# Kernel tuning notes

Measured on AMD Instinct MI355X. Metric: run time of the kernel, lower is better.

Reference implementation:

```python
import jax, jax.numpy as jnp
import numpy as np

G, A = 512, 24            # graphs, atoms per graph (constant -> static edge count)
N, E = G * A, G * A * A   # nodes, fully-connected edges per graph (incl. self loops)
HID, TDIM, BB, NFREQ, NLAYER = 128, 256, 64, 10, 4
DIS = NFREQ * 2 * 3                     # SinusoidsEmbedding dim = 60
EDGE_IN = 2 * HID + 6 + DIS             # 322
LAT_IN = HID + 16 + TDIM                # 400


def setup_inputs() -> dict:
    key = jax.random.key(0)
    ks = jax.random.split(key, 32)
    s = 0.02

    # block-diagonal fully-connected edge list (dense_to_sparse of ones(A,A) per graph)
    local = np.arange(A)
    off = np.repeat(np.arange(G) * A, A * A)
    e0 = np.tile(np.repeat(local, A), G) + off   # row index
    e1 = np.tile(np.tile(local, A), G) + off     # col index
    edge_index = jnp.asarray(np.stack([e0, e1]), dtype=jnp.int32)

    inp = {
        "t": jax.random.normal(ks[0], (G, TDIM), jnp.float32),
        "bb_embs": jax.random.normal(ks[1], (N, BB), jnp.float32),
        "frac_coords": jax.random.uniform(ks[2], (N, 3), jnp.float32),
        "so3_vecs": jax.random.normal(ks[3], (N, 16), jnp.float32),
        "lattices": jax.random.normal(ks[4], (G, 6), jnp.float32),
        "num_atoms": jnp.full((G,), A, dtype=jnp.int32),
        "node2graph": jnp.repeat(jnp.arange(G, dtype=jnp.int32), A),
        "edge_index": edge_index,
        # parameters
        "W_emb": jax.random.normal(ks[5], (BB, HID)) * s,
        "b_emb": jnp.zeros((HID,), jnp.float32),
        "W_lat": jax.random.normal(ks[6], (LAT_IN, HID)) * s,
        "b_lat": jnp.zeros((HID,), jnp.float32),
        "We1": jax.random.normal(ks[7], (NLAYER, EDGE_IN, HID)) * s,
        "be1": jnp.zeros((NLAYER, HID), jnp.float32),
        "We2": jax.random.normal(ks[8], (NLAYER, HID, HID)) * s,
        "be2": jnp.zeros((NLAYER, HID), jnp.float32),
        "Wn1": jax.random.normal(ks[9], (NLAYER, 2 * HID, HID)) * s,
        "bn1": jnp.zeros((NLAYER, HID), jnp.float32),
        "Wn2": jax.random.normal(ks[10], (NLAYER, HID, HID)) * s,
        "bn2": jnp.zeros((NLAYER, HID), jnp.float32),
        "W_coord": jax.random.normal(ks[11], (HID, 3)) * s,
        "W_lattice": jax.random.normal(ks[12], (HID, 6)) * s,
        "W_so3": jax.random.normal(ks[13], (HID, 4)) * s,
    }
    return inp


def reference(t, bb_embs, frac_coords, so3_vecs, lattices, num_atoms, node2graph,
              edge_index, W_emb, b_emb, W_lat, b_lat,
              We1, be1, We2, be2, Wn1, bn1, Wn2, bn2,
              W_coord, W_lattice, W_so3):
    n_nodes = bb_embs.shape[0]
    n_graphs = t.shape[0]
    e0, e1 = edge_index[0], edge_index[1]

    # gen_edges (period == 1): frac_diff = (x_j - x_i) % 1
    frac_diff = jnp.mod(frac_coords[e1] - frac_coords[e0], 1.0)
    # SinusoidsEmbedding (detached in torch)
    freqs = 2.0 * jnp.pi * jnp.arange(NFREQ, dtype=frac_diff.dtype)
    ang = (frac_diff[:, :, None] * freqs).reshape(-1, 3 * NFREQ)   # [E, 30]
    pe = jax.lax.stop_gradient(jnp.concatenate([jnp.sin(ang), jnp.cos(ang)], -1))  # [E, 60]

    edge2graph = node2graph[e0]
    lat_e = lattices[edge2graph]                                   # [E, 6]

    # node embedding + latent projection (no activation on atom_latent_emb)
    h0 = jnp.concatenate([bb_embs @ W_emb + b_emb, so3_vecs, t[node2graph]], axis=1)
    h = h0 @ W_lat + b_lat                                          # [N, HID]

    counts = jax.ops.segment_sum(jnp.ones((e0.shape[0], 1), h.dtype), e0,
                                 num_segments=n_nodes)
    counts = jnp.maximum(counts, 1.0)

    def csp_layer(h, p):
        we1, b1, we2, b2, wn1, c1, wn2, c2 = p
        ein = jnp.concatenate([h[e0], h[e1], lat_e, pe], axis=1)    # [E, 322]
        ef = jax.nn.silu(jax.nn.silu(ein @ we1 + b1) @ we2 + b2)    # [E, HID]
        agg = jax.ops.segment_sum(ef, e0, num_segments=n_nodes) / counts  # mean
        nin = jnp.concatenate([h, agg], axis=1)                     # [N, 2*HID]
        out = jax.nn.silu(jax.nn.silu(nin @ wn1 + c1) @ wn2 + c2)
        return h + out, None

    h, _ = jax.lax.scan(csp_layer, h, (We1, be1, We2, be2, Wn1, bn1, Wn2, bn2))

    coord_out = h @ W_coord                                          # [N, 3]
    so3_out = h @ W_so3
    so3_out = so3_out / jnp.linalg.norm(so3_out, axis=-1, keepdims=True)

    gcounts = jax.ops.segment_sum(jnp.ones((n_nodes, 1), h.dtype), node2graph,
                                  num_segments=n_graphs)
    gfeat = jax.ops.segment_sum(h, node2graph, num_segments=n_graphs) / gcounts
    lattice_out = gfeat @ W_lattice                                  # [G, 6]

    # back2interval (period == 1) applied to coord_out + frac_coords
    return (lattice_out, jnp.mod(coord_out + frac_coords, 1.0), so3_out)
```

## Files before the change

### kernel.cpp

```cpp
#include <hip/hip_runtime.h>
#include <hip/hip_bf16.h>


#define NG 512
#define NA 24
#define HID 128
#define TDIM 256
#define NBB 64
#define TPB 256
#define LFRAGS 208
#define OFF_A 0
#define OFF_B 32
#define OFF_D 64
#define OFF_E2 80
#define OFF_N1 112
#define OFF_N2 176

typedef __bf16 bf16x8 __attribute__((ext_vector_type(8)));
typedef float  f32x4  __attribute__((ext_vector_type(4)));

#define O_HB   0
#define O_BAUG 6528
#define O_AGG  14720
#define O_PE   21248
#define O_MID  35072
#define O_TL   61184
#define O_FRAC 61696
#define O_LAT6 61984
#define SMEM_BYTES 62016

__device__ __forceinline__ float silu_f(float x) { return x / (1.0f + __expf(-x)); }

__device__ __forceinline__ unsigned short cvtbf(float x) {
    __hip_bfloat16 b = __float2bfloat16(x);
    return *reinterpret_cast<unsigned short*>(&b);
}

__device__ __forceinline__ f32x4 MFMA(bf16x8 a, bf16x8 b, f32x4 c) {
    return __builtin_amdgcn_mfma_f32_16x16x32_bf16(a, b, c, 0, 0, 0);
}

__device__ __forceinline__ bf16x8 gfrag(const unsigned short* ws, int fragIdx, int l) {
    const int4* p = reinterpret_cast<const int4*>(ws + (size_t)fragIdx * 512) + l;
    return __builtin_bit_cast(bf16x8, *p);
}
__device__ __forceinline__ bf16x8 lfrag(const unsigned short* buf, int stride, int row0, int kofs, int l) {
    const int4* p = reinterpret_cast<const int4*>(buf + (row0 + (l & 15)) * stride + kofs + ((l >> 4) << 3));
    return __builtin_bit_cast(bf16x8, *p);
}
__device__ __forceinline__ bf16x8 lfragRaw(const unsigned short* buf, int fragIdx, int l) {
    const int4* p = reinterpret_cast<const int4*>(buf + fragIdx * 512) + l;
    return __builtin_bit_cast(bf16x8, *p);
}
__device__ __forceinline__ bf16x8 augfrag(int row, int q) {
    int i0l = row / 24;
    int ja  = row - i0l * 24;
    int k2  = 4 + ja;
    bf16x8 v;
#pragma unroll
    for (int e = 0; e < 8; ++e) {
        int k = q * 8 + e;
        bool one = (k == i0l) || (k == k2) || (k == 28);
        v[e] = one ? (__bf16)1.0f : (__bf16)0.0f;
    }
    return v;
}

#define FMA4(ACC, S, W) { (ACC).x += (S)*(W).x; (ACC).y += (S)*(W).y; \
                          (ACC).z += (S)*(W).z; (ACC).w += (S)*(W).w; }

__device__ __forceinline__ float4 ld4(const float* __restrict__ p) {
    return *reinterpret_cast<const float4*>(p);
}

__global__ void __launch_bounds__(TPB) pack_weights(
    const float* __restrict__ We1, const float* __restrict__ We2,
    const float* __restrict__ Wn1, const float* __restrict__ Wn2,
    unsigned short* __restrict__ ws)
{
    int w = blockIdx.x * 4 + (threadIdx.x >> 6);
    int l = threadIdx.x & 63;
    int q = l >> 4, c16 = l & 15;
    int layer = w / LFRAGS, r = w % LFRAGS;
    const float* src; int K4, seg, klim; bool isPE = false;
    if (r < 32)       { seg = 0;   K4 = 4; src = We1 + (size_t)layer*322*128;           klim = 128; }
    else if (r < 64)  { seg = 32;  K4 = 4; src = We1 + (size_t)layer*322*128 + 128*128; klim = 128; }
    else if (r < 80)  { seg = 64;  K4 = 2; src = We1 + (size_t)layer*322*128 + 262*128; klim = 60; isPE = true; }
    else if (r < 112) { seg = 80;  K4 = 4; src = We2 + (size_t)layer*128*128;           klim = 128; }
    else if (r < 176) { seg = 112; K4 = 8; src = Wn1 + (size_t)layer*256*128;           klim = 256; }
    else              { seg = 176; K4 = 4; src = Wn2 + (size_t)layer*128*128;           klim = 128; }
    int rr = r - seg; int nt = rr / K4, ks = rr % K4;
    unsigned short vals[8];
#pragma unroll
    for (int j = 0; j < 8; ++j) {
        int row = ks * 32 + q * 8 + j;
        float v = 0.f;
        if (row < klim) {
            int srow = row;
            if (isPE) {
                int d = row / 20, t = row % 20, sc = t / 10, f = t % 10;
                srow = sc * 30 + d * 10 + f;
            }
            v = src[(size_t)srow * 128 + nt * 16 + c16];
        }
        vals[j] = cvtbf(v);
    }
    unsigned int d0 = (unsigned)vals[0] | ((unsigned)vals[1] << 16);
    unsigned int d1 = (unsigned)vals[2] | ((unsigned)vals[3] << 16);
    unsigned int d2 = (unsigned)vals[4] | ((unsigned)vals[5] << 16);
    unsigned int d3 = (unsigned)vals[6] | ((unsigned)vals[7] << 16);
    int4 o = make_int4((int)d0, (int)d1, (int)d2, (int)d3);
    *reinterpret_cast<int4*>(ws + ((size_t)w * 64 + l) * 8) = o;
}

__global__ void __launch_bounds__(TPB, 2) cspnet_mfma(
    const float* __restrict__ t_in, const float* __restrict__ bb_embs,
    const float* __restrict__ frac, const float* __restrict__ so3,
    const float* __restrict__ lattices,
    const float* __restrict__ W_emb, const float* __restrict__ b_emb,
    const float* __restrict__ W_lat, const float* __restrict__ b_lat,
    const float* __restrict__ We1, const float* __restrict__ be1,
    const float* __restrict__ be2, const float* __restrict__ bn1,
    const float* __restrict__ bn2,
    const float* __restrict__ W_coord, const float* __restrict__ W_lattice,
    const float* __restrict__ W_so3,
    const unsigned short* __restrict__ wsU,
    float* __restrict__ out)
{
    __shared__ __align__(16) char smem[SMEM_BYTES];
    unsigned short* hbU   = (unsigned short*)(smem + O_HB);
    unsigned short* baugU = (unsigned short*)(smem + O_BAUG);
    unsigned short* aggU  = (unsigned short*)(smem + O_AGG);
    unsigned short* peU   = (unsigned short*)(smem + O_PE);
    unsigned short* midU  = (unsigned short*)(smem + O_MID);
    unsigned short* t1U   = midU;
    float* tlS   = (float*)(smem + O_TL);
    float* fracS = (float*)(smem + O_FRAC);
    float* lat6S = (float*)(smem + O_LAT6);
    float* embS  = (float*)(smem + O_MID);
    float* hscrF = (float*)(smem + O_PE);

    const int g   = blockIdx.x;
    const int tid = threadIdx.x;
    const int l   = tid & 63;
    const int wv  = tid >> 6;
    const int q   = l >> 4;
    const int c16 = l & 15;
    const float inv24 = 1.0f / 24.0f;
    const f32x4 FZ = {0.f, 0.f, 0.f, 0.f};

    if (tid < NA * 3) {
        int i = tid / 3, d = tid - i * 3;
        fracS[i * 3 + d] = frac[(size_t)(g * NA + i) * 3 + d];
    }
    if (tid < 6) lat6S[tid] = lattices[(size_t)g * 6 + tid];
    for (int v = tid; v < 384; v += TPB) {
        int ct = v / 48, rest = v % 48, cl = rest / 3, jp = 5 + rest % 3;
        baugU[ct * 512 + (48 + cl) * 8 + jp] = 0;
    }

    {
        const int cg = tid & 31, rg = tid >> 5, c0 = cg * 4;
        float4 acc[3];
        float4 be = ld4(b_emb + c0);
        acc[0] = be; acc[1] = be; acc[2] = be;
        const float* bbg = bb_embs + (size_t)(g * NA) * NBB;
#pragma unroll 4
        for (int k = 0; k < NBB; ++k) {
            float4 w = ld4(W_emb + (size_t)k * HID + c0);
            float b0v = bbg[rg * NBB + k];
            float b1v = bbg[(rg + 8) * NBB + k];
            float b2v = bbg[(rg + 16) * NBB + k];
            FMA4(acc[0], b0v, w); FMA4(acc[1], b1v, w); FMA4(acc[2], b2v, w);
        }
#pragma unroll
        for (int s = 0; s < 3; ++s)
            *reinterpret_cast<float4*>(&embS[(rg + 8 * s) * HID + c0]) = acc[s];
    }
    if (tid < HID) {
        float acc = 0.f;
        const float* tg = t_in + (size_t)g * TDIM;
        for (int k = 0; k < TDIM; ++k)
            acc += tg[k] * W_lat[(size_t)(144 + k) * HID + tid];
        tlS[tid] = acc;
    }
    __syncthreads();

    {
        const int cg = tid & 31, rg = tid >> 5, c0 = cg * 4;
        float4 acc[3];
        float4 bl = ld4(b_lat + c0);
        float4 tv = *reinterpret_cast<const float4*>(tlS + c0);
        bl.x += tv.x; bl.y += tv.y; bl.z += tv.z; bl.w += tv.w;
        acc[0] = bl; acc[1] = bl; acc[2] = bl;
#pragma unroll 4
        for (int k = 0; k < HID; ++k) {
            float4 w = ld4(W_lat + (size_t)k * HID + c0);
            float e0 = embS[rg * HID + k], e1 = embS[(rg + 8) * HID + k], e2 = embS[(rg + 16) * HID + k];
            FMA4(acc[0], e0, w); FMA4(acc[1], e1, w); FMA4(acc[2], e2, w);
        }
        const float* so3g = so3 + (size_t)(g * NA) * 16;
#pragma unroll
        for (int k = 0; k < 16; ++k) {
            float4 w = ld4(W_lat + (size_t)(HID + k) * HID + c0);
            float s0 = so3g[rg * 16 + k], s1 = so3g[(rg + 8) * 16 + k], s2 = so3g[(rg + 16) * 16 + k];
            FMA4(acc[0], s0, w); FMA4(acc[1], s1, w); FMA4(acc[2], s2, w);
        }
#pragma unroll
        for (int s = 0; s < 3; ++s) {
            int row = rg + 8 * s;
            *reinterpret_cast<float4*>(&hscrF[row * HID + c0]) = acc[s];
            ushort4 v = make_ushort4(cvtbf(acc[s].x), cvtbf(acc[s].y), cvtbf(acc[s].z), cvtbf(acc[s].w));
            *reinterpret_cast<ushort4*>(&hbU[row * 136 + c0]) = v;
        }
    }
    __syncthreads();

    float hreg[2][2][4];
#pragma unroll
    for (int ctl = 0; ctl < 2; ++ctl)
#pragma unroll
        for (int rt = 0; rt < 2; ++rt) {
            int row = rt * 16 + c16;
#pragma unroll
            for (int r = 0; r < 4; ++r)
                hreg[ctl][rt][r] = (row < 24) ? hscrF[row * HID + (wv * 2 + ctl) * 16 + q * 4 + r] : 0.f;
        }
    __syncthreads();
    for (int v = tid; v < 384; v += TPB) {
        int row = v >> 2, c = 60 + (v & 3);
        peU[row * 72 + c] = 0;
    }

    for (int ly = 0; ly < 4; ++ly) {
        const int LOFF = ly * LFRAGS;
        const float* be1_l = be1 + ly * HID;
        const float* We1_l = We1 + (size_t)ly * 322 * HID;
        const float* be2_l = be2 + ly * HID;
        const float* bn1_l = bn1 + ly * HID;
        const float* bn2_l = bn2 + ly * HID;

        bf16x8 w1dr[4][2];
#pragma unroll
        for (int ctl = 0; ctl < 4; ++ctl)
#pragma unroll
            for (int ks = 0; ks < 2; ++ks)
                w1dr[ctl][ks] = gfrag(wsU, LOFF + OFF_D + ((wv & 1) * 4 + ctl) * 2 + ks, l);
        bf16x8 we2r[4][4];
#pragma unroll
        for (int ntl = 0; ntl < 4; ++ntl)
#pragma unroll
            for (int ks = 0; ks < 4; ++ks)
                we2r[ntl][ks] = gfrag(wsU, LOFF + OFF_E2 + ((wv & 1) * 4 + ntl) * 4 + ks, l);
        float be2r[4];
#pragma unroll
        for (int ntl = 0; ntl < 4; ++ntl)
            be2r[ntl] = be2_l[((wv & 1) * 4 + ntl) * 16 + c16];

        {
            f32x4 pacc[2][2];
#pragma unroll
            for (int a = 0; a < 2; ++a) { pacc[a][0] = FZ; pacc[a][1] = FZ; }
#pragma unroll
            for (int ks = 0; ks < 4; ++ks) {
                bf16x8 b0 = lfrag(hbU, 136, 0, ks * 32, l);
                bf16x8 b1 = lfrag(hbU, 136, 16, ks * 32, l);
#pragma unroll
                for (int ctl = 0; ctl < 2; ++ctl) {
                    bf16x8 a = gfrag(wsU, LOFF + OFF_B + (wv * 2 + ctl) * 4 + ks, l);
                    pacc[ctl][0] = MFMA(a, b0, pacc[ctl][0]);
                    pacc[ctl][1] = MFMA(a, b1, pacc[ctl][1]);
                }
            }
#pragma unroll
            for (int ctl = 0; ctl < 2; ++ctl)
#pragma unroll
                for (int rt = 0; rt < 2; ++rt) {
                    int row = rt * 16 + c16;
                    if (row < 24) {
                        int ka = 4 + row, qp = ka >> 3, jp = ka & 7;
#pragma unroll
                        for (int r = 0; r < 4; ++r) {
                            int c = (wv * 2 + ctl) * 16 + q * 4 + r;
                            baugU[(c >> 4) * 512 + (qp * 16 + (c & 15)) * 8 + jp] = cvtbf(pacc[ctl][rt][r]);
                        }
                    }
                }
        }
        if (tid < HID) {
            float a = be1_l[tid];
#pragma unroll
            for (int k = 0; k < 6; ++k)
                a += lat6S[k] * We1_l[(size_t)(256 + k) * HID + tid];
            int c = tid;
            baugU[(c >> 4) * 512 + (48 + (c & 15)) * 8 + 4] = cvtbf(a);
        }
        __syncthreads();

        for (int ck = 0; ck < 6; ++ck) {
            for (int v = tid; v < 288; v += TPB) {
                int row = v / 3, d = v - row * 3;
                int i0l = row / 24, ja = row - i0l * 24;
                float fd = fracS[ja * 3 + d] - fracS[(ck * 4 + i0l) * 3 + d];
                fd -= floorf(fd);
                float sv[20];
#pragma unroll
                for (int f = 0; f < 10; ++f) {
                    float ang = fd * (6.2831853071795864f * (float)f);
                    sv[f] = __sinf(ang); sv[10 + f] = __cosf(ang);
                }
                unsigned short* dst = peU + row * 72 + d * 20;
#pragma unroll
                for (int m = 0; m < 5; ++m) {
                    ushort4 pk = make_ushort4(cvtbf(sv[m*4]), cvtbf(sv[m*4+1]), cvtbf(sv[m*4+2]), cvtbf(sv[m*4+3]));
                    *reinterpret_cast<ushort4*>(dst + m * 4) = pk;
                }
            }
            {
                f32x4 hacc[2] = {FZ, FZ};
#pragma unroll
                for (int ks = 0; ks < 4; ++ks) {
                    bf16x8 b = lfrag(hbU, 136, ck * 4, ks * 32, l);
#pragma unroll
                    for (int ctl = 0; ctl < 2; ++ctl) {
                        bf16x8 a = gfrag(wsU, LOFF + OFF_A + (wv * 2 + ctl) * 4 + ks, l);
                        hacc[ctl] = MFMA(a, b, hacc[ctl]);
                    }
                }
                if (c16 < 4) {
#pragma unroll
                    for (int ctl = 0; ctl < 2; ++ctl)
#pragma unroll
                        for (int r = 0; r < 4; ++r) {
                            int c = (wv * 2 + ctl) * 16 + q * 4 + r;
                            baugU[(c >> 4) * 512 + (c & 15) * 8 + c16] = cvtbf(hacc[ctl][r]);
                        }
                }
            }
            __syncthreads();

            {
                const int ct0 = (wv & 1) * 4;
                const int rt0 = (wv >> 1) * 3;
                f32x4 macc[4][3];
#pragma unroll
                for (int a = 0; a < 4; ++a)
#pragma unroll
                    for (int b = 0; b < 3; ++b) macc[a][b] = FZ;
#pragma unroll
                for (int ks = 0; ks < 2; ++ks) {
                    bf16x8 bb[3];
#pragma unroll
                    for (int rtl = 0; rtl < 3; ++rtl)
                        bb[rtl] = lfrag(peU, 72, (rt0 + rtl) * 16, ks * 32, l);
#pragma unroll
                    for (int ctl = 0; ctl < 4; ++ctl)
#pragma unroll
                        for (int rtl = 0; rtl < 3; ++rtl)
                            macc[ctl][rtl] = MFMA(w1dr[ctl][ks], bb[rtl], macc[ctl][rtl]);
                }
                {
                    bf16x8 ab[3];
#pragma unroll
                    for (int rtl = 0; rtl < 3; ++rtl)
                        ab[rtl] = augfrag((rt0 + rtl) * 16 + c16, q);
#pragma unroll
                    for (int ctl = 0; ctl < 4; ++ctl) {
                        bf16x8 a2 = lfragRaw(baugU, ct0 + ctl, l);
#pragma unroll
                        for (int rtl = 0; rtl < 3; ++rtl)
                            macc[ctl][rtl] = MFMA(a2, ab[rtl], macc[ctl][rtl]);
                    }
                }
#pragma unroll
                for (int ctl = 0; ctl < 4; ++ctl)
#pragma unroll
                    for (int rtl = 0; rtl < 3; ++rtl) {
                        int row = (rt0 + rtl) * 16 + c16;
                        int cb = (ct0 + ctl) * 16 + q * 4;
                        ushort4 v = make_ushort4(cvtbf(silu_f(macc[ctl][rtl][0])),
                                                 cvtbf(silu_f(macc[ctl][rtl][1])),
                                                 cvtbf(silu_f(macc[ctl][rtl][2])),
                                                 cvtbf(silu_f(macc[ctl][rtl][3])));
                        *reinterpret_cast<ushort4*>(&midU[row * 136 + cb]) = v;
                    }
            }
            __syncthreads();

            {
                const int mh = wv >> 1;
                f32x4 eacc[3][4];
#pragma unroll
                for (int a = 0; a < 3; ++a)
#pragma unroll
                    for (int b = 0; b < 4; ++b) eacc[a][b] = FZ;
#pragma unroll
                for (int mtl = 0; mtl < 3; ++mtl) {
                    bf16x8 am[4];
#pragma unroll
                    for (int ks = 0; ks < 4; ++ks)
                        am[ks] = lfrag(midU, 136, (3 * mh + mtl) * 16, ks * 32, l);
#pragma unroll
                    for (int ntl = 0; ntl < 4; ++ntl)
#pragma unroll
                        for (int ks = 0; ks < 4; ++ks)
                            eacc[mtl][ntl] = MFMA(am[ks], we2r[ntl][ks], eacc[mtl][ntl]);
                }
#pragma unroll
                for (int ntl = 0; ntl < 4; ++ntl) {
                    float s0 = 0.f, s1 = 0.f;
#pragma unroll
                    for (int r = 0; r < 4; ++r) {
                        float e0 = silu_f(eacc[0][ntl][r] + be2r[ntl]);
                        float e1 = silu_f(eacc[1][ntl][r] + be2r[ntl]);
                        float e2 = silu_f(eacc[2][ntl][r] + be2r[ntl]);
                        s0 += e0; s1 += e2;
                        if (q < 2) s0 += e1; else s1 += e1;
                    }
                    s0 += __shfl_xor(s0, 16, 64); s0 += __shfl_xor(s0, 32, 64);
                    s1 += __shfl_xor(s1, 16, 64); s1 += __shfl_xor(s1, 32, 64);
                    if (q == 0) {
                        int i0a = ck * 4 + 2 * mh;
                        int cc = ((wv & 1) * 4 + ntl) * 16 + c16;
                        aggU[i0a * 136 + cc]       = cvtbf(s0 * inv24);
                        aggU[(i0a + 1) * 136 + cc] = cvtbf(s1 * inv24);
                    }
                }
            }
            __syncthreads();
        }

        {
            f32x4 t1a[2][2];
#pragma unroll
            for (int a = 0; a < 2; ++a) { t1a[a][0] = FZ; t1a[a][1] = FZ; }
#pragma unroll
            for (int ks = 0; ks < 8; ++ks) {
                bf16x8 b0, b1;
                if (ks < 4) { b0 = lfrag(hbU, 136, 0, ks * 32, l);  b1 = lfrag(hbU, 136, 16, ks * 32, l); }
                else        { b0 = lfrag(aggU, 136, 0, (ks - 4) * 32, l); b1 = lfrag(aggU, 136, 16, (ks - 4) * 32, l); }
#pragma unroll
                for (int ctl = 0; ctl < 2; ++ctl) {
                    bf16x8 a = gfrag(wsU, LOFF + OFF_N1 + (wv * 2 + ctl) * 8 + ks, l);
                    t1a[ctl][0] = MFMA(a, b0, t1a[ctl][0]);
                    t1a[ctl][1] = MFMA(a, b1, t1a[ctl][1]);
                }
            }
            float bn1r[2][4];
#pragma unroll
            for (int ctl = 0; ctl < 2; ++ctl)
#pragma unroll
                for (int r = 0; r < 4; ++r)
                    bn1r[ctl][r] = bn1_l[(wv * 2 + ctl) * 16 + q * 4 + r];
#pragma unroll
            for (int ctl = 0; ctl < 2; ++ctl)
#pragma unroll
                for (int rt = 0; rt < 2; ++rt) {
                    int row = rt * 16 + c16;
                    int cb = (wv * 2 + ctl) * 16 + q * 4;
                    ushort4 v = make_ushort4(cvtbf(silu_f(t1a[ctl][rt][0] + bn1r[ctl][0])),
                                             cvtbf(silu_f(t1a[ctl][rt][1] + bn1r[ctl][1])),
                                             cvtbf(silu_f(t1a[ctl][rt][2] + bn1r[ctl][2])),
                                             cvtbf(silu_f(t1a[ctl][rt][3] + bn1r[ctl][3])));
                    *reinterpret_cast<ushort4*>(&t1U[row * 136 + cb]) = v;
                }
        }
        __syncthreads();
        {
            f32x4 t2a[2][2];
#pragma unroll
            for (int a = 0; a < 2; ++a) { t2a[a][0] = FZ; t2a[a][1] = FZ; }
#pragma unroll
            for (int ks = 0; ks < 4; ++ks) {
                bf16x8 b0 = lfrag(t1U, 136, 0, ks * 32, l);
                bf16x8 b1 = lfrag(t1U, 136, 16, ks * 32, l);
#pragma unroll
                for (int ctl = 0; ctl < 2; ++ctl) {
                    bf16x8 a = gfrag(wsU, LOFF + OFF_N2 + (wv * 2 + ctl) * 4 + ks, l);
                    t2a[ctl][0] = MFMA(a, b0, t2a[ctl][0]);
                    t2a[ctl][1] = MFMA(a, b1, t2a[ctl][1]);
                }
            }
            float bn2r[2][4];
#pragma unroll
            for (int ctl = 0; ctl < 2; ++ctl)
#pragma unroll
                for (int r = 0; r < 4; ++r)
                    bn2r[ctl][r] = bn2_l[(wv * 2 + ctl) * 16 + q * 4 + r];
#pragma unroll
            for (int ctl = 0; ctl < 2; ++ctl)
#pragma unroll
                for (int rt = 0; rt < 2; ++rt) {
                    int row = rt * 16 + c16;
#pragma unroll
                    for (int r = 0; r < 4; ++r)
                        hreg[ctl][rt][r] += silu_f(t2a[ctl][rt][r] + bn2r[ctl][r]);
                    if (row < 24) {
                        int cb = (wv * 2 + ctl) * 16 + q * 4;
                        ushort4 v = make_ushort4(cvtbf(hreg[ctl][rt][0]), cvtbf(hreg[ctl][rt][1]),
                                                 cvtbf(hreg[ctl][rt][2]), cvtbf(hreg[ctl][rt][3]));
                        *reinterpret_cast<ushort4*>(&hbU[row * 136 + cb]) = v;
                    }
                }
        }
        __syncthreads();
    }

#pragma unroll
    for (int ctl = 0; ctl < 2; ++ctl)
#pragma unroll
        for (int rt = 0; rt < 2; ++rt) {
            int row = rt * 16 + c16;
            if (row < 24) {
                float4 v = make_float4(hreg[ctl][rt][0], hreg[ctl][rt][1], hreg[ctl][rt][2], hreg[ctl][rt][3]);
                *reinterpret_cast<float4*>(&hscrF[row * HID + (wv * 2 + ctl) * 16 + q * 4]) = v;
            }
        }
    __syncthreads();

    if (tid < HID) {
        float s = 0.f;
#pragma unroll 4
        for (int i = 0; i < NA; ++i) s += hscrF[i * HID + tid];
        tlS[tid] = s * inv24;
    }
    if (tid < NA * 3) {
        int i = tid / 3, d = tid - i * 3;
        float acc = 0.f;
#pragma unroll 4
        for (int k = 0; k < HID; ++k) acc += hscrF[i * HID + k] * W_coord[k * 3 + d];
        acc += fracS[i * 3 + d];
        acc -= floorf(acc);
        out[(size_t)NG * 6 + (size_t)(g * NA + i) * 3 + d] = acc;
    }
    if (tid < NA) {
        int i = tid;
        float v0 = 0.f, v1 = 0.f, v2 = 0.f, v3 = 0.f;
#pragma unroll 4
        for (int k = 0; k < HID; ++k) {
            float hv = hscrF[i * HID + k];
            v0 += hv * W_so3[k * 4 + 0]; v1 += hv * W_so3[k * 4 + 1];
            v2 += hv * W_so3[k * 4 + 2]; v3 += hv * W_so3[k * 4 + 3];
        }
        float inv = 1.0f / sqrtf(v0 * v0 + v1 * v1 + v2 * v2 + v3 * v3);
        size_t o = (size_t)NG * 6 + (size_t)NG * NA * 3 + (size_t)(g * NA + i) * 4;
        out[o + 0] = v0 * inv; out[o + 1] = v1 * inv;
        out[o + 2] = v2 * inv; out[o + 3] = v3 * inv;
    }
    __syncthreads();
    if (tid < 6) {
        float acc = 0.f;
#pragma unroll 4
        for (int c = 0; c < HID; ++c) acc += tlS[c] * W_lattice[c * 6 + tid];
        out[(size_t)g * 6 + tid] = acc;
    }
}

extern "C" void kernel_launch(void* const* d_in, const int* in_sizes, int n_in,
                              void* d_out, int out_size, void* d_ws, size_t ws_size,
                              hipStream_t stream) {
    const float* t_in    = (const float*)d_in[0];
    const float* bb      = (const float*)d_in[1];
    const float* frac    = (const float*)d_in[2];
    const float* so3     = (const float*)d_in[3];
    const float* lat     = (const float*)d_in[4];
    const float* W_emb   = (const float*)d_in[8];
    const float* b_emb   = (const float*)d_in[9];
    const float* W_lat   = (const float*)d_in[10];
    const float* b_lat   = (const float*)d_in[11];
    const float* We1     = (const float*)d_in[12];
    const float* be1     = (const float*)d_in[13];
    const float* We2     = (const float*)d_in[14];
    const float* be2     = (const float*)d_in[15];
    const float* Wn1     = (const float*)d_in[16];
    const float* bn1     = (const float*)d_in[17];
    const float* Wn2     = (const float*)d_in[18];
    const float* bn2     = (const float*)d_in[19];
    const float* W_coord = (const float*)d_in[20];
    const float* W_latt  = (const float*)d_in[21];
    const float* W_so3   = (const float*)d_in[22];

    unsigned short* ws = (unsigned short*)d_ws;
    hipLaunchKernelGGL(pack_weights, dim3(208), dim3(TPB), 0, stream,
                       We1, We2, Wn1, Wn2, ws);
    hipLaunchKernelGGL(cspnet_mfma, dim3(NG), dim3(TPB), 0, stream,
                       t_in, bb, frac, so3, lat, W_emb, b_emb, W_lat, b_lat,
                       We1, be1, be2, bn1, bn2, W_coord, W_latt, W_so3,
                       (const unsigned short*)ws, (float*)d_out);
}
```

Measured before the change: 372.9 us.

## Compute PE fragments in registers, precompute time projection, cut LDS for occupancy

Generates the sinusoid positional-encoding B fragments directly in registers with the hardware sin instruction (turns expressed as offsets) and reorders the packed PE weights to match, removing the peU LDS buffer and its write/read passes. The t@W_lat projection moves into extra blocks of the pack kernel, written to workspace when it is large enough. Shared memory shrinks so launch bounds can allow 3 blocks per CU. It also hoists the OFF_A weight fragments and aug fragments, and switches to a faster rcp-based silu and a bit-trick bf16 packing. Risks are register pressure at the higher occupancy target, bf16 rounding differences (no NaN handling), and sin accuracy from the hardware instruction.

```diff
diff --git a/kernel.cpp b/kernel.cpp
--- a/kernel.cpp
+++ b/kernel.cpp
@@ -15,6 +15,8 @@
 #define OFF_E2 80
 #define OFF_N1 112
 #define OFF_N2 176
+#define FRAG_BYTES (832ull * 1024ull)
+#define TL_BYTES   (512ull * 128ull * 4ull)
 
 typedef __bf16 bf16x8 __attribute__((ext_vector_type(8)));
 typedef float  f32x4  __attribute__((ext_vector_type(4)));
@@ -22,18 +24,25 @@
 #define O_HB   0
 #define O_BAUG 6528
 #define O_AGG  14720
-#define O_PE   21248
-#define O_MID  35072
-#define O_TL   61184
-#define O_FRAC 61696
-#define O_LAT6 61984
-#define SMEM_BYTES 62016
-
-__device__ __forceinline__ float silu_f(float x) { return x / (1.0f + __expf(-x)); }
+#define O_MID  21248
+#define O_TL   47360
+#define O_FRAC 47872
+#define O_LAT6 48160
+#define SMEM_BYTES 48192
+
+__device__ __forceinline__ float silu_f(float x) {
+    return x * __builtin_amdgcn_rcpf(1.0f + __expf(-x));
+}
 
 __device__ __forceinline__ unsigned short cvtbf(float x) {
     __hip_bfloat16 b = __float2bfloat16(x);
     return *reinterpret_cast<unsigned short*>(&b);
+}
+
+__device__ __forceinline__ unsigned pk2(float a, float b) {
+    unsigned ua = __builtin_bit_cast(unsigned, a) + 0x8000u;
+    unsigned ub = __builtin_bit_cast(unsigned, b) + 0x8000u;
+    return __builtin_amdgcn_perm(ub, ua, 0x07060302u);
 }
 
 __device__ __forceinline__ f32x4 MFMA(bf16x8 a, bf16x8 b, f32x4 c) {
@@ -76,8 +85,25 @@
 __global__ void __launch_bounds__(TPB) pack_weights(
     const float* __restrict__ We1, const float* __restrict__ We2,
     const float* __restrict__ Wn1, const float* __restrict__ Wn2,
-    unsigned short* __restrict__ ws)
+    const float* __restrict__ t_in, const float* __restrict__ W_lat,
+    unsigned short* __restrict__ ws, float* __restrict__ tlAll, int useTl)
 {
+    if (blockIdx.x >= 208) {
+        if (!useTl) return;
+        int b2 = blockIdx.x - 208;
+        int gl = threadIdx.x >> 5, lane32 = threadIdx.x & 31;
+        int g = b2 * 8 + gl, c0 = lane32 * 4;
+        float4 acc = make_float4(0.f, 0.f, 0.f, 0.f);
+        const float* tg = t_in + (size_t)g * TDIM;
+#pragma unroll 4
+        for (int k = 0; k < TDIM; ++k) {
+            float tv = tg[k];
+            float4 w = ld4(W_lat + (size_t)(144 + k) * HID + c0);
+            FMA4(acc, tv, w);
+        }
+        *reinterpret_cast<float4*>(tlAll + (size_t)g * HID + c0) = acc;
+        return;
+    }
     int w = blockIdx.x * 4 + (threadIdx.x >> 6);
     int l = threadIdx.x & 63;
     int q = l >> 4, c16 = l & 15;
@@ -85,7 +111,7 @@
     const float* src; int K4, seg, klim; bool isPE = false;
     if (r < 32)       { seg = 0;   K4 = 4; src = We1 + (size_t)layer*322*128;           klim = 128; }
     else if (r < 64)  { seg = 32;  K4 = 4; src = We1 + (size_t)layer*322*128 + 128*128; klim = 128; }
-    else if (r < 80)  { seg = 64;  K4 = 2; src = We1 + (size_t)layer*322*128 + 262*128; klim = 60; isPE = true; }
+    else if (r < 80)  { seg = 64;  K4 = 2; src = We1 + (size_t)layer*322*128 + 262*128; klim = 64; isPE = true; }
     else if (r < 112) { seg = 80;  K4 = 4; src = We2 + (size_t)layer*128*128;           klim = 128; }
     else if (r < 176) { seg = 112; K4 = 8; src = Wn1 + (size_t)layer*256*128;           klim = 256; }
     else              { seg = 176; K4 = 4; src = Wn2 + (size_t)layer*128*128;           klim = 128; }
@@ -96,12 +122,24 @@
         int row = ks * 32 + q * 8 + j;
         float v = 0.f;
         if (row < klim) {
-            int srow = row;
             if (isPE) {
-                int d = row / 20, t = row % 20, sc = t / 10, f = t % 10;
-                srow = sc * 30 + d * 10 + f;
-            }
-            v = src[(size_t)srow * 128 + nt * 16 + c16];
+                int gI = row >> 3, e = row & 7;
+                int d = 0, trig = 0, f = 0; bool valid = true;
+                if (gI < 6) { d = gI % 3; trig = gI / 3; f = e; }
+                else if (gI == 6) {
+                    const int dt[8] = {0,0,1,1,2,2,0,0};
+                    const int tt[8] = {0,0,0,0,0,0,1,1};
+                    const int ft[8] = {8,9,8,9,8,9,8,9};
+                    d = dt[e]; trig = tt[e]; f = ft[e];
+                } else {
+                    if (e < 4) { const int dt[4] = {1,1,2,2}; const int ft[4] = {8,9,8,9};
+                                 d = dt[e]; trig = 1; f = ft[e]; }
+                    else valid = false;
+                }
+                if (valid) v = src[(size_t)(trig * 30 + d * 10 + f) * 128 + nt * 16 + c16];
+            } else {
+                v = src[(size_t)row * 128 + nt * 16 + c16];
+            }
         }
         vals[j] = cvtbf(v);
     }
@@ -113,7 +151,7 @@
     *reinterpret_cast<int4*>(ws + ((size_t)w * 64 + l) * 8) = o;
 }
 
-__global__ void __launch_bounds__(TPB, 2) cspnet_mfma(
+__global__ void __launch_bounds__(TPB, 3) cspnet_mfma(
     const float* __restrict__ t_in, const float* __restrict__ bb_embs,
     const float* __restrict__ frac, const float* __restrict__ so3,
     const float* __restrict__ lattices,
@@ -124,21 +162,20 @@
     const float* __restrict__ bn2,
     const float* __restrict__ W_coord, const float* __restrict__ W_lattice,
     const float* __restrict__ W_so3,
-    const unsigned short* __restrict__ wsU,
-    float* __restrict__ out)
+    const unsigned short* __restrict__ wsU, const float* __restrict__ tlAll,
+    int useTl, float* __restrict__ out)
 {
     __shared__ __align__(16) char smem[SMEM_BYTES];
     unsigned short* hbU   = (unsigned short*)(smem + O_HB);
     unsigned short* baugU = (unsigned short*)(smem + O_BAUG);
     unsigned short* aggU  = (unsigned short*)(smem + O_AGG);
-    unsigned short* peU   = (unsigned short*)(smem + O_PE);
     unsigned short* midU  = (unsigned short*)(smem + O_MID);
     unsigned short* t1U   = midU;
     float* tlS   = (float*)(smem + O_TL);
     float* fracS = (float*)(smem + O_FRAC);
     float* lat6S = (float*)(smem + O_LAT6);
     float* embS  = (float*)(smem + O_MID);
-    float* hscrF = (float*)(smem + O_PE);
+    float* hscrF = (float*)(smem + O_MID + 12288);
 
     const int g   = blockIdx.x;
     const int tid = threadIdx.x;
@@ -146,6 +183,7 @@
     const int wv  = tid >> 6;
     const int q   = l >> 4;
     const int c16 = l & 15;
+    const int mh  = wv >> 1;
     const float inv24 = 1.0f / 24.0f;
     const f32x4 FZ = {0.f, 0.f, 0.f, 0.f};
 
@@ -157,6 +195,15 @@
     for (int v = tid; v < 384; v += TPB) {
         int ct = v / 48, rest = v % 48, cl = rest / 3, jp = 5 + rest % 3;
         baugU[ct * 512 + (48 + cl) * 8 + jp] = 0;
+    }
+    if (useTl) {
+        if (tid < HID) tlS[tid] = tlAll[(size_t)g * HID + tid];
+    } else if (tid < HID) {
+        float acc = 0.f;
+        const float* tg = t_in + (size_t)g * TDIM;
+        for (int k = 0; k < TDIM; ++k)
+            acc += tg[k] * W_lat[(size_t)(144 + k) * HID + tid];
+        tlS[tid] = acc;
     }
 
     {
@@ -177,13 +224,6 @@
         for (int s = 0; s < 3; ++s)
             *reinterpret_cast<float4*>(&embS[(rg + 8 * s) * HID + c0]) = acc[s];
     }
-    if (tid < HID) {
-        float acc = 0.f;
-        const float* tg = t_in + (size_t)g * TDIM;
-        for (int k = 0; k < TDIM; ++k)
-            acc += tg[k] * W_lat[(size_t)(144 + k) * HID + tid];
-        tlS[tid] = acc;
-    }
     __syncthreads();
 
     {
@@ -210,8 +250,8 @@
         for (int s = 0; s < 3; ++s) {
             int row = rg + 8 * s;
             *reinterpret_cast<float4*>(&hscrF[row * HID + c0]) = acc[s];
-            ushort4 v = make_ushort4(cvtbf(acc[s].x), cvtbf(acc[s].y), cvtbf(acc[s].z), cvtbf(acc[s].w));
-            *reinterpret_cast<ushort4*>(&hbU[row * 136 + c0]) = v;
+            uint2 pv = make_uint2(pk2(acc[s].x, acc[s].y), pk2(acc[s].z, acc[s].w));
+            *reinterpret_cast<uint2*>(&hbU[row * 136 + c0]) = pv;
         }
     }
     __syncthreads();
@@ -227,10 +267,11 @@
                 hreg[ctl][rt][r] = (row < 24) ? hscrF[row * HID + (wv * 2 + ctl) * 16 + q * 4 + r] : 0.f;
         }
     __syncthreads();
-    for (int v = tid; v < 384; v += TPB) {
-        int row = v >> 2, c = 60 + (v & 3);
-        peU[row * 72 + c] = 0;
-    }
+
+    bf16x8 augB[3];
+#pragma unroll
+    for (int rtl = 0; rtl < 3; ++rtl)
+        augB[rtl] = augfrag((mh * 3 + rtl) * 16 + c16, q);
 
     for (int ly = 0; ly < 4; ++ly) {
         const int LOFF = ly * LFRAGS;
@@ -298,34 +339,76 @@
         __syncthreads();
 
         for (int ck = 0; ck < 6; ++ck) {
-            for (int v = tid; v < 288; v += TPB) {
-                int row = v / 3, d = v - row * 3;
-                int i0l = row / 24, ja = row - i0l * 24;
-                float fd = fracS[ja * 3 + d] - fracS[(ck * 4 + i0l) * 3 + d];
-                fd -= floorf(fd);
-                float sv[20];
-#pragma unroll
-                for (int f = 0; f < 10; ++f) {
-                    float ang = fd * (6.2831853071795864f * (float)f);
-                    sv[f] = __sinf(ang); sv[10 + f] = __cosf(ang);
-                }
-                unsigned short* dst = peU + row * 72 + d * 20;
-#pragma unroll
-                for (int m = 0; m < 5; ++m) {
-                    ushort4 pk = make_ushort4(cvtbf(sv[m*4]), cvtbf(sv[m*4+1]), cvtbf(sv[m*4+2]), cvtbf(sv[m*4+3]));
-                    *reinterpret_cast<ushort4*>(dst + m * 4) = pk;
-                }
-            }
+            bf16x8 oa[2][4];
+#pragma unroll
+            for (int ctl = 0; ctl < 2; ++ctl)
+#pragma unroll
+                for (int ks = 0; ks < 4; ++ks)
+                    oa[ctl][ks] = gfrag(wsU, LOFF + OFF_A + (wv * 2 + ctl) * 4 + ks, l);
+
+            bf16x8 peF[3][2];
+#pragma unroll
+            for (int rtl = 0; rtl < 3; ++rtl) {
+                int r = (mh * 3 + rtl) * 16 + c16;
+                int i0l = (r * 43) >> 10;
+                int j = r - i0l * 24;
+                int i0 = ck * 4 + i0l;
+                float fd0 = fracS[j * 3 + 0] - fracS[i0 * 3 + 0];
+                float fd1 = fracS[j * 3 + 1] - fracS[i0 * 3 + 1];
+                float fd2 = fracS[j * 3 + 2] - fracS[i0 * 3 + 2];
+                {
+                    float fsel = (q == 1) ? fd1 : fd0;
+                    fsel = (q == 2) ? fd2 : fsel;
+                    float toff = (q == 3) ? 0.25f : 0.0f;
+                    unsigned p[4];
+#pragma unroll
+                    for (int ep = 0; ep < 4; ++ep) {
+                        float v0 = __builtin_amdgcn_sinf(fsel * (float)(2 * ep) + toff);
+                        float v1 = __builtin_amdgcn_sinf(fsel * (float)(2 * ep + 1) + toff);
+                        p[ep] = pk2(v0, v1);
+                    }
+                    peF[rtl][0] = __builtin_bit_cast(bf16x8, make_int4(p[0], p[1], p[2], p[3]));
+                }
+                {
+                    float fsel = (q == 0) ? fd1 : fd2;
+                    unsigned p[4];
+#pragma unroll
+                    for (int ep = 0; ep < 4; ++ep) {
+                        float vv[2];
+#pragma unroll
+                        for (int hh = 0; hh < 2; ++hh) {
+                            int e = 2 * ep + hh;
+                            const int   d6[8] = {0,0,1,1,2,2,0,0};
+                            const float f6[8] = {8.f,9.f,8.f,9.f,8.f,9.f,8.f,9.f};
+                            const float t6[8] = {0,0,0,0,0,0,0.25f,0.25f};
+                            float tdef = fsel * (float)e + 0.25f;
+                            float fd6 = (d6[e] == 0) ? fd0 : ((d6[e] == 1) ? fd1 : fd2);
+                            float t2 = fd6 * f6[e] + t6[e];
+                            float t3 = 0.0f;
+                            if (e < 4) {
+                                const int   d7[4] = {1,1,2,2};
+                                const float f7[4] = {8.f,9.f,8.f,9.f};
+                                float fd7 = (d7[e] == 1) ? fd1 : fd2;
+                                t3 = fd7 * f7[e] + 0.25f;
+                            }
+                            float t = (q == 2) ? t2 : tdef;
+                            t = (q == 3) ? t3 : t;
+                            vv[hh] = __builtin_amdgcn_sinf(t);
+                        }
+                        p[ep] = pk2(vv[0], vv[1]);
+                    }
+                    peF[rtl][1] = __builtin_bit_cast(bf16x8, make_int4(p[0], p[1], p[2], p[3]));
+                }
+            }
+
             {
                 f32x4 hacc[2] = {FZ, FZ};
 #pragma unroll
                 for (int ks = 0; ks < 4; ++ks) {
                     bf16x8 b = lfrag(hbU, 136, ck * 4, ks * 32, l);
 #pragma unroll
-                    for (int ctl = 0; ctl < 2; ++ctl) {
-                        bf16x8 a = gfrag(wsU, LOFF + OFF_A + (wv * 2 + ctl) * 4 + ks, l);
-                        hacc[ctl] = MFMA(a, b, hacc[ctl]);
-                    }
+                    for (int ctl = 0; ctl < 2; ++ctl)
+                        hacc[ctl] = MFMA(oa[ctl][ks], b, hacc[ctl]);
                 }
                 if (c16 < 4) {
 #pragma unroll
@@ -341,54 +424,39 @@
 
             {
                 const int ct0 = (wv & 1) * 4;
-                const int rt0 = (wv >> 1) * 3;
                 f32x4 macc[4][3];
 #pragma unroll
                 for (int a = 0; a < 4; ++a)
 #pragma unroll
                     for (int b = 0; b < 3; ++b) macc[a][b] = FZ;
 #pragma unroll
-                for (int ks = 0; ks < 2; ++ks) {
-                    bf16x8 bb[3];
+                for (int ks = 0; ks < 2; ++ks)
+#pragma unroll
+                    for (int ctl = 0; ctl < 4; ++ctl)
+#pragma unroll
+                        for (int rtl = 0; rtl < 3; ++rtl)
+                            macc[ctl][rtl] = MFMA(w1dr[ctl][ks], peF[rtl][ks], macc[ctl][rtl]);
+#pragma unroll
+                for (int ctl = 0; ctl < 4; ++ctl) {
+                    bf16x8 a2 = lfragRaw(baugU, ct0 + ctl, l);
 #pragma unroll
                     for (int rtl = 0; rtl < 3; ++rtl)
-                        bb[rtl] = lfrag(peU, 72, (rt0 + rtl) * 16, ks * 32, l);
-#pragma unroll
-                    for (int ctl = 0; ctl < 4; ++ctl)
-#pragma unroll
-                        for (int rtl = 0; rtl < 3; ++rtl)
-                            macc[ctl][rtl] = MFMA(w1dr[ctl][ks], bb[rtl], macc[ctl][rtl]);
-                }
-                {
-                    bf16x8 ab[3];
-#pragma unroll
-                    for (int rtl = 0; rtl < 3; ++rtl)
-                        ab[rtl] = augfrag((rt0 + rtl) * 16 + c16, q);
-#pragma unroll
-                    for (int ctl = 0; ctl < 4; ++ctl) {
-                        bf16x8 a2 = lfragRaw(baugU, ct0 + ctl, l);
-#pragma unroll
-                        for (int rtl = 0; rtl < 3; ++rtl)
-                            macc[ctl][rtl] = MFMA(a2, ab[rtl], macc[ctl][rtl]);
+                        macc[ctl][rtl] = MFMA(a2, augB[rtl], macc[ctl][rtl]);
+                }
+#pragma unroll
+                for (int ctl = 0; ctl < 4; ++ctl)
+#pragma unroll
+                    for (int rtl = 0; rtl < 3; ++rtl) {
+                        int row = (mh * 3 + rtl) * 16 + c16;
+                        int cb = (ct0 + ctl) * 16 + q * 4;
+                        uint2 pv = make_uint2(pk2(silu_f(macc[ctl][rtl][0]), silu_f(macc[ctl][rtl][1])),
+                                              pk2(silu_f(macc[ctl][rtl][2]), silu_f(macc[ctl][rtl][3])));
+                        *reinterpret_cast<uint2*>(&midU[row * 136 + cb]) = pv;
                     }
-                }
-#pragma unroll
-                for (int ctl = 0; ctl < 4; ++ctl)
-#pragma unroll
-                    for (int rtl = 0; rtl < 3; ++rtl) {
-                        int row = (rt0 + rtl) * 16 + c16;
-                        int cb = (ct0 + ctl) * 16 + q * 4;
-                        ushort4 v = make_ushort4(cvtbf(silu_f(macc[ctl][rtl][0])),
-                                                 cvtbf(silu_f(macc[ctl][rtl][1])),
-                                                 cvtbf(silu_f(macc[ctl][rtl][2])),
-                                                 cvtbf(silu_f(macc[ctl][rtl][3])));
-                        *reinterpret_cast<ushort4*>(&midU[row * 136 + cb]) = v;
-                    }
             }
             __syncthreads();
 
             {
-                const int mh = wv >> 1;
                 f32x4 eacc[3][4];
 #pragma unroll
                 for (int a = 0; a < 3; ++a)
@@ -458,11 +526,11 @@
                 for (int rt = 0; rt < 2; ++rt) {
                     int row = rt * 16 + c16;
                     int cb = (wv * 2 + ctl) * 16 + q * 4;
-                    ushort4 v = make_ushort4(cvtbf(silu_f(t1a[ctl][rt][0] + bn1r[ctl][0])),
-                                             cvtbf(silu_f(t1a[ctl][rt][1] + bn1r[ctl][1])),
-                                             cvtbf(silu_f(t1a[ctl][rt][2] + bn1r[ctl][2])),
-                                             cvtbf(silu_f(t1a[ctl][rt][3] + bn1r[ctl][3])));
-                    *reinterpret_cast<ushort4*>(&t1U[row * 136 + cb]) = v;
+                    uint2 pv = make_uint2(pk2(silu_f(t1a[ctl][rt][0] + bn1r[ctl][0]),
+                                              silu_f(t1a[ctl][rt][1] + bn1r[ctl][1])),
+                                          pk2(silu_f(t1a[ctl][rt][2] + bn1r[ctl][2]),
+                                              silu_f(t1a[ctl][rt][3] + bn1r[ctl][3])));
+                    *reinterpret_cast<uint2*>(&t1U[row * 136 + cb]) = pv;
                 }
         }
         __syncthreads();
@@ -497,9 +565,9 @@
                         hreg[ctl][rt][r] += silu_f(t2a[ctl][rt][r] + bn2r[ctl][r]);
                     if (row < 24) {
                         int cb = (wv * 2 + ctl) * 16 + q * 4;
-                        ushort4 v = make_ushort4(cvtbf(hreg[ctl][rt][0]), cvtbf(hreg[ctl][rt][1]),
-                                                 cvtbf(hreg[ctl][rt][2]), cvtbf(hreg[ctl][rt][3]));
-                        *reinterpret_cast<ushort4*>(&hbU[row * 136 + cb]) = v;
+                        uint2 pv = make_uint2(pk2(hreg[ctl][rt][0], hreg[ctl][rt][1]),
+                                              pk2(hreg[ctl][rt][2], hreg[ctl][rt][3]));
+                        *reinterpret_cast<uint2*>(&hbU[row * 136 + cb]) = pv;
                     }
                 }
         }
@@ -581,10 +649,14 @@
     const float* W_so3   = (const float*)d_in[22];
 
     unsigned short* ws = (unsigned short*)d_ws;
-    hipLaunchKernelGGL(pack_weights, dim3(208), dim3(TPB), 0, stream,
-                       We1, We2, Wn1, Wn2, ws);
+    float* tlAll = (float*)((char*)d_ws + FRAG_BYTES);
+    int useTl = (ws_size >= FRAG_BYTES + TL_BYTES) ? 1 : 0;
+
+    hipLaunchKernelGGL(pack_weights, dim3(272), dim3(TPB), 0, stream,
+                       We1, We2, Wn1, Wn2, t_in, W_lat, ws, tlAll, useTl);
     hipLaunchKernelGGL(cspnet_mfma, dim3(NG), dim3(TPB), 0, stream,
                        t_in, bb, frac, so3, lat, W_emb, b_emb, W_lat, b_lat,
                        We1, be1, be2, bn1, bn2, W_coord, W_latt, W_so3,
-                       (const unsigned short*)ws, (float*)d_out);
-}
+                       (const unsigned short*)ws, (const float*)tlAll, useTl,
+                       (float*)d_out);
+}
```

Measured after the change: 456.8 us. +22.5%, slower.
